# Optimization experiments

Hardware: AMD Instinct MI355X
Metric: run time of the kernel (lower is better)

Reference implementation:

```python
import jax, jax.numpy as jnp
import numpy as np

N_HEADS, D_MODEL, D_HEAD = 16, 1024, 64
BATCH, SEQ = 2, 2048
INIT_RANGE = 0.02


def setup_inputs() -> dict:
    key = jax.random.key(0)
    ks = jax.random.split(key, 5)
    x = jax.random.normal(ks[0], (BATCH, SEQ, D_MODEL), dtype=jnp.float32)
    W_Q = jax.random.normal(ks[1], (N_HEADS, D_MODEL, D_HEAD), dtype=jnp.float32) * INIT_RANGE
    W_K = jax.random.normal(ks[2], (N_HEADS, D_MODEL, D_HEAD), dtype=jnp.float32) * INIT_RANGE
    W_V = jax.random.normal(ks[3], (N_HEADS, D_MODEL, D_HEAD), dtype=jnp.float32) * INIT_RANGE
    W_O = jax.random.normal(ks[4], (N_HEADS, D_HEAD, D_MODEL), dtype=jnp.float32) * INIT_RANGE
    b_Q = jnp.zeros((N_HEADS, D_HEAD), dtype=jnp.float32)
    b_K = jnp.zeros((N_HEADS, D_HEAD), dtype=jnp.float32)
    b_V = jnp.zeros((N_HEADS, D_HEAD), dtype=jnp.float32)
    b_O = jnp.zeros((D_MODEL,), dtype=jnp.float32)
    return {"normalized_resid_pre": x, "W_Q": W_Q, "W_K": W_K, "W_V": W_V,
            "W_O": W_O, "b_Q": b_Q, "b_K": b_K, "b_V": b_V, "b_O": b_O}


def reference(normalized_resid_pre, W_Q, W_K, W_V, W_O, b_Q, b_K, b_V, b_O):
    x = normalized_resid_pre  # [b, s, d_model]
    q = jnp.einsum('bsm,hmd->bshd', x, W_Q) + b_Q  # [b, s, h, d_head]
    k = jnp.einsum('bsm,hmd->bshd', x, W_K) + b_K
    v = jnp.einsum('bsm,hmd->bshd', x, W_V) + b_V
    scores = jnp.einsum('bqhd,bkhd->bhqk', q, k) / jnp.sqrt(jnp.float32(D_HEAD))
    seq = x.shape[1]
    causal = jnp.tril(jnp.ones((seq, seq), dtype=bool))  # True where allowed
    scores = jnp.where(causal, scores, jnp.float32(-jnp.inf))
    pattern = jax.nn.softmax(scores, axis=-1)  # [b, h, q, k]
    z = jnp.einsum('bhqk,bkhd->bqhd', pattern, v)
    attn_out = jnp.einsum('bqhd,hdm->bqm', z, W_O) + b_O
    return attn_out
```

## Files before the change

kernel.cpp:

```cpp
#include <hip/hip_runtime.h>
#include <hip/hip_bf16.h>

#define BATCH 2
#define SEQL 2048
#define NH 16
#define DH 64
#define DM 1024
#define QSCALE 0.1803368801111244f

typedef __hip_bfloat16 bf16;
typedef __attribute__((ext_vector_type(8)))  short bf16x8;
typedef __attribute__((ext_vector_type(4)))  float f32x4;
typedef __attribute__((ext_vector_type(16))) float f32x16;

__device__ __forceinline__ void gl_lds16(const void* g, void* l) {
    __builtin_amdgcn_global_load_lds(
        (const __attribute__((address_space(1))) unsigned int*)g,
        (__attribute__((address_space(3))) unsigned int*)l, 16, 0, 0);
}

__device__ __forceinline__ unsigned int pkbf(float a, float b) {
    union { bf16 h[2]; unsigned int u; } x;
    x.h[0] = __float2bfloat16(a); x.h[1] = __float2bfloat16(b);
    return x.u;
}

__global__ __launch_bounds__(256) void prep_kernel(
    const float* __restrict__ x,
    const float* __restrict__ Wq, const float* __restrict__ Wk,
    const float* __restrict__ Wv, const float* __restrict__ Wo,
    bf16* __restrict__ Wt, bf16* __restrict__ xb)
{
    const int zi = blockIdx.z;
    if (zi == 4) {
        const int bid = blockIdx.y * 16 + blockIdx.x;
        const size_t base = ((size_t)bid * 256 + threadIdx.x) * 4;
        #pragma unroll
        for (int it = 0; it < 16; ++it) {
            const size_t i = base + (size_t)it * 262144;
            const float4 v = *(const float4*)(x + i);
            bf16 o[4];
            o[0] = __float2bfloat16(v.x); o[1] = __float2bfloat16(v.y);
            o[2] = __float2bfloat16(v.z); o[3] = __float2bfloat16(v.w);
            *(uint2*)(xb + i) = *(const uint2*)o;
        }
        return;
    }

    __shared__ float ts[64][65];
    const float* src = (zi == 0) ? Wq : (zi == 1) ? Wk : (zi == 2) ? Wv : Wo;
    bf16* dst = Wt + (size_t)zi * DM * DM;
    const int row0 = blockIdx.y * 64;
    const int col0 = blockIdx.x * 64;
    const int tx = threadIdx.x & 63;
    const int ty = threadIdx.x >> 6;

    if (zi < 3) {
        const int h = col0 >> 6;
        #pragma unroll
        for (int i = 0; i < 16; ++i) {
            const int r = ty + 4 * i;
            ts[r][tx] = src[h * (DM * DH) + (row0 + r) * DH + tx];
        }
    } else {
        #pragma unroll
        for (int i = 0; i < 16; ++i) {
            const int r = ty + 4 * i;
            ts[r][tx] = src[(size_t)(row0 + r) * DM + col0 + tx];
        }
    }
    __syncthreads();
    #pragma unroll
    for (int i = 0; i < 16; ++i) {
        const int rr = ty + 4 * i;
        dst[(size_t)(col0 + rr) * DM + row0 + tx] = __float2bfloat16(ts[tx][rr]);
    }
}

__global__ __launch_bounds__(256) void qkv_gemm(
    const bf16* __restrict__ xb, const bf16* __restrict__ Wt,
    const float* __restrict__ bq, const float* __restrict__ bk, const float* __restrict__ bv,
    bf16* __restrict__ qkv)
{
    __shared__ __align__(16) bf16 As[2][128 * 32];
    __shared__ __align__(16) bf16 Bs[2][128 * 32];

    const int t = threadIdx.x;
    const int lane = t & 63, w = t >> 6;
    const int ml = lane & 15, quad = lane >> 4;
    const int wr = w >> 1, wc = w & 1;
    const int bn = blockIdx.x, bm = blockIdx.y, which = blockIdx.z;

    const bf16* A0 = xb + (size_t)(bm * 128) * DM;
    const bf16* B0 = Wt + (size_t)which * DM * DM + (size_t)(bn * 128) * DM;
    const float* bias = (which == 0) ? bq : (which == 1) ? bk : bv;
    bf16* outb = qkv + (size_t)which * (BATCH * SEQL * NH * DH);
    const float oscale = (which == 0) ? QSCALE : 1.0f;

    f32x4 acc[4][4];
    #pragma unroll
    for (int i = 0; i < 4; ++i)
        #pragma unroll
        for (int j = 0; j < 4; ++j) acc[i][j] = (f32x4){0.f, 0.f, 0.f, 0.f};

    const int r0 = t >> 2, c0 = (t & 3) * 8;
    const int f1 = t + 256;
    const int r1 = f1 >> 2, c1 = (f1 & 3) * 8;

    for (int kt = 0; kt < DM / 64; ++kt) {
        const int k0 = kt * 64;
        __syncthreads();
        #pragma unroll
        for (int half = 0; half < 2; ++half) {
            const int kh = k0 + half * 32;
            gl_lds16(A0 + (size_t)r0 * DM + kh + c0, &As[half][t * 8]);
            gl_lds16(A0 + (size_t)r1 * DM + kh + c1, &As[half][f1 * 8]);
            gl_lds16(B0 + (size_t)r0 * DM + kh + c0, &Bs[half][t * 8]);
            gl_lds16(B0 + (size_t)r1 * DM + kh + c1, &Bs[half][f1 * 8]);
        }
        __syncthreads();
        #pragma unroll
        for (int half = 0; half < 2; ++half) {
            bf16x8 af[4], bfr[4];
            #pragma unroll
            for (int i = 0; i < 4; ++i)
                af[i] = *(const bf16x8*)&As[half][(wr * 64 + i * 16 + ml) * 32 + quad * 8];
            #pragma unroll
            for (int j = 0; j < 4; ++j)
                bfr[j] = *(const bf16x8*)&Bs[half][(wc * 64 + j * 16 + ml) * 32 + quad * 8];
            #pragma unroll
            for (int i = 0; i < 4; ++i)
                #pragma unroll
                for (int j = 0; j < 4; ++j)
                    acc[i][j] = __builtin_amdgcn_mfma_f32_16x16x32_bf16(af[i], bfr[j], acc[i][j], 0, 0, 0);
        }
    }

    float bb[4];
    #pragma unroll
    for (int j = 0; j < 4; ++j) bb[j] = bias[bn * 128 + wc * 64 + j * 16 + ml];

    if (which == 2) {
        #pragma unroll
        for (int i = 0; i < 4; ++i) {
            const int row0v = bm * 128 + wr * 64 + i * 16 + quad * 4;
            const int b = row0v >> 11;
            const int s0 = row0v & (SEQL - 1);
            #pragma unroll
            for (int j = 0; j < 4; ++j) {
                const int col = bn * 128 + wc * 64 + j * 16 + ml;
                const int h = col >> 6, d = col & 63;
                bf16 tmp[4];
                #pragma unroll
                for (int rg = 0; rg < 4; ++rg)
                    tmp[rg] = __float2bfloat16(acc[i][j][rg] + bb[j]);
                *(uint2*)&outb[(((size_t)(b * NH + h)) * DH + d) * SEQL + s0] =
                    *(const uint2*)tmp;
            }
        }
    } else {
        #pragma unroll
        for (int i = 0; i < 4; ++i) {
            #pragma unroll
            for (int rg = 0; rg < 4; ++rg) {
                const int row = bm * 128 + wr * 64 + i * 16 + quad * 4 + rg;
                const int b = row >> 11;
                const int s = row & (SEQL - 1);
                #pragma unroll
                for (int j = 0; j < 4; ++j) {
                    const int col = bn * 128 + wc * 64 + j * 16 + ml;
                    const int h = col >> 6, d = col & 63;
                    outb[(((size_t)(b * NH + h)) * SEQL + s) * DH + d] =
                        __float2bfloat16((acc[i][j][rg] + bb[j]) * oscale);
                }
            }
        }
    }
}

__global__ __launch_bounds__(256) void oproj_gemm(
    const bf16* __restrict__ zb, const bf16* __restrict__ Bt,
    const float* __restrict__ bo, float* __restrict__ out)
{
    __shared__ __align__(16) bf16 As[2][128 * 32];
    __shared__ __align__(16) bf16 Bs[2][64 * 32];

    const int t = threadIdx.x;
    const int lane = t & 63, w = t >> 6;
    const int ml = lane & 15, quad = lane >> 4;
    const int wr = w >> 1, wc = w & 1;
    const int bn = blockIdx.x, bm = blockIdx.y;

    const bf16* A0 = zb + (size_t)(bm * 128) * DM;
    const bf16* B0 = Bt + (size_t)(bn * 64) * DM;

    f32x4 acc[4][2];
    #pragma unroll
    for (int i = 0; i < 4; ++i)
        #pragma unroll
        for (int j = 0; j < 2; ++j) acc[i][j] = (f32x4){0.f, 0.f, 0.f, 0.f};

    const int r0 = t >> 2, c0 = (t & 3) * 8;
    const int f1 = t + 256;
    const int r1 = f1 >> 2, c1 = (f1 & 3) * 8;

    for (int kt = 0; kt < DM / 64; ++kt) {
        const int k0 = kt * 64;
        __syncthreads();
        #pragma unroll
        for (int half = 0; half < 2; ++half) {
            const int kh = k0 + half * 32;
            gl_lds16(A0 + (size_t)r0 * DM + kh + c0, &As[half][t * 8]);
            gl_lds16(A0 + (size_t)r1 * DM + kh + c1, &As[half][f1 * 8]);
            gl_lds16(B0 + (size_t)r0 * DM + kh + c0, &Bs[half][t * 8]);
        }
        __syncthreads();
        #pragma unroll
        for (int half = 0; half < 2; ++half) {
            bf16x8 af[4], bfr[2];
            #pragma unroll
            for (int i = 0; i < 4; ++i)
                af[i] = *(const bf16x8*)&As[half][(wr * 64 + i * 16 + ml) * 32 + quad * 8];
            #pragma unroll
            for (int j = 0; j < 2; ++j)
                bfr[j] = *(const bf16x8*)&Bs[half][(wc * 32 + j * 16 + ml) * 32 + quad * 8];
            #pragma unroll
            for (int i = 0; i < 4; ++i)
                #pragma unroll
                for (int j = 0; j < 2; ++j)
                    acc[i][j] = __builtin_amdgcn_mfma_f32_16x16x32_bf16(af[i], bfr[j], acc[i][j], 0, 0, 0);
        }
    }

    float bb[2];
    #pragma unroll
    for (int j = 0; j < 2; ++j) bb[j] = bo[bn * 64 + wc * 32 + j * 16 + ml];

    #pragma unroll
    for (int i = 0; i < 4; ++i) {
        #pragma unroll
        for (int rg = 0; rg < 4; ++rg) {
            const int row = bm * 128 + wr * 64 + i * 16 + quad * 4 + rg;
            #pragma unroll
            for (int j = 0; j < 2; ++j) {
                const int col = bn * 64 + wc * 32 + j * 16 + ml;
                out[(size_t)row * DM + col] = acc[i][j][rg] + bb[j];
            }
        }
    }
}

__global__ __launch_bounds__(256) void attn_kernel(
    const bf16* __restrict__ qg, const bf16* __restrict__ kg, const bf16* __restrict__ vtg,
    bf16* __restrict__ z)
{
    __shared__ __align__(16) bf16 KsS[2][64 * 64];
    __shared__ __align__(16) bf16 VtS[2][64 * 64];

    const int t    = threadIdx.x;
    const int lane = t & 63;
    const int w    = t >> 6;
    const int q5   = lane & 31;
    const int hl   = lane >> 5;
    const int qgr  = w & 1;
    const int kvg  = w >> 1;

    const int bh = blockIdx.x;
    const int b  = bh >> 4;
    const int h  = bh & 15;
    const int qt = (gridDim.y - 1) - blockIdx.y;
    const int q0 = qt * 64;

    const size_t base   = (size_t)bh * SEQL * DH;
    const size_t vtbase = (size_t)bh * DH * SEQL;

    const int s0 = t, s1 = t + 256;
    const int r0s = s0 >> 3, c0s = (s0 & 7) ^ (r0s & 7);
    const int r1s = s1 >> 3, c1s = (s1 & 7) ^ (r1s & 7);

    bf16x8 aq[4];
    {
        const bf16* qp = qg + base + (size_t)(q0 + qgr * 32 + q5) * DH;
        #pragma unroll
        for (int c = 0; c < 4; ++c)
            aq[c] = *(const bf16x8*)(qp + c * 16 + hl * 8);
    }

    f32x16 zacc[2];
    #pragma unroll
    for (int dg = 0; dg < 2; ++dg)
        #pragma unroll
        for (int r = 0; r < 16; ++r) zacc[dg][r] = 0.f;
    float lacc = 0.f;

    gl_lds16(kg + base + (size_t)r0s * DH + c0s * 8, &KsS[0][s0 * 8]);
    gl_lds16(kg + base + (size_t)r1s * DH + c1s * 8, &KsS[0][s1 * 8]);
    gl_lds16(vtg + vtbase + (size_t)r0s * SEQL + c0s * 8, &VtS[0][s0 * 8]);
    gl_lds16(vtg + vtbase + (size_t)r1s * SEQL + c1s * 8, &VtS[0][s1 * 8]);

    for (int kt = 0; kt <= qt; ++kt) {
        const int cur = kt & 1;
        __syncthreads();

        if (kt < qt) {
            const int kc = (kt + 1) * 64;
            bf16* Kd = &KsS[cur ^ 1][0];
            bf16* Vd = &VtS[cur ^ 1][0];
            gl_lds16(kg + base + (size_t)(kc + r0s) * DH + c0s * 8, Kd + s0 * 8);
            gl_lds16(kg + base + (size_t)(kc + r1s) * DH + c1s * 8, Kd + s1 * 8);
            gl_lds16(vtg + vtbase + (size_t)r0s * SEQL + kc + c0s * 8, Vd + s0 * 8);
            gl_lds16(vtg + vtbase + (size_t)r1s * SEQL + kc + c1s * 8, Vd + s1 * 8);
        }

        if (kt == qt && kvg == 1 && qgr == 0) continue;

        const bf16* Ks = &KsS[cur][0];
        const bf16* Vt = &VtS[cur][0];

        f32x16 sc;
        #pragma unroll
        for (int r = 0; r < 16; ++r) sc[r] = 0.f;
        {
            const int row = kvg * 32 + q5;
            const int rx  = row & 7;
            __builtin_amdgcn_s_setprio(1);
            #pragma unroll
            for (int s = 0; s < 4; ++s) {
                const int cc = (s * 2 + hl) ^ rx;
                const bf16x8 ak = *(const bf16x8*)(&Ks[row * 64 + cc * 8]);
                sc = __builtin_amdgcn_mfma_f32_32x32x16_bf16(ak, aq[s], sc, 0, 0, 0);
            }
            __builtin_amdgcn_s_setprio(0);
        }

        if (kt == qt && kvg == qgr) {
            #pragma unroll
            for (int r = 0; r < 16; ++r) {
                const int kvloc = (r & 3) + 8 * (r >> 2) + 4 * hl;
                sc[r] = (kvloc > q5) ? -1e30f : sc[r];
            }
        }

        unsigned int wpk[8];
        #pragma unroll
        for (int g = 0; g < 4; ++g) {
            const float p0 = __builtin_exp2f(sc[4 * g + 0]);
            const float p1 = __builtin_exp2f(sc[4 * g + 1]);
            const float p2 = __builtin_exp2f(sc[4 * g + 2]);
            const float p3 = __builtin_exp2f(sc[4 * g + 3]);
            lacc += (p0 + p1) + (p2 + p3);
            wpk[2 * g + 0] = pkbf(p0, p1);
            wpk[2 * g + 1] = pkbf(p2, p3);
        }

        bf16x8 pf[2];
        #pragma unroll
        for (int ks = 0; ks < 2; ++ks) {
            const unsigned int S0 = hl ? wpk[4 * ks + 0] : wpk[4 * ks + 2];
            const unsigned int S1 = hl ? wpk[4 * ks + 1] : wpk[4 * ks + 3];
            const unsigned int R0 = __shfl_xor((int)S0, 32);
            const unsigned int R1 = __shfl_xor((int)S1, 32);
            union { unsigned int u[4]; bf16x8 v; } f;
            f.u[0] = hl ? R0 : wpk[4 * ks + 0];
            f.u[1] = hl ? R1 : wpk[4 * ks + 1];
            f.u[2] = hl ? wpk[4 * ks + 2] : R0;
            f.u[3] = hl ? wpk[4 * ks + 3] : R1;
            pf[ks] = f.v;
        }

        __builtin_amdgcn_s_setprio(1);
        #pragma unroll
        for (int dg = 0; dg < 2; ++dg) {
            const int row = dg * 32 + q5;
            const int rx  = row & 7;
            #pragma unroll
            for (int ks = 0; ks < 2; ++ks) {
                const int cc = (kvg * 4 + ks * 2 + hl) ^ rx;
                const bf16x8 av = *(const bf16x8*)(&Vt[row * 64 + cc * 8]);
                zacc[dg] = __builtin_amdgcn_mfma_f32_32x32x16_bf16(av, pf[ks], zacc[dg], 0, 0, 0);
            }
        }
        __builtin_amdgcn_s_setprio(0);
    }

    __syncthreads();
    if (kvg == 1) {
        float* sp = (qgr == 0) ? (float*)KsS : (float*)VtS;
        #pragma unroll
        for (int dg = 0; dg < 2; ++dg)
            #pragma unroll
            for (int r = 0; r < 16; ++r)
                sp[(dg * 16 + r) * 64 + lane] = zacc[dg][r];
        sp[2048 + lane] = lacc;
    }
    __syncthreads();
    if (kvg == 0) {
        const float* sp = (qgr == 0) ? (const float*)KsS : (const float*)VtS;
        #pragma unroll
        for (int dg = 0; dg < 2; ++dg)
            #pragma unroll
            for (int r = 0; r < 16; ++r)
                zacc[dg][r] += sp[(dg * 16 + r) * 64 + lane];
        lacc += sp[2048 + lane];
        lacc += __shfl_xor(lacc, 32);
        const float invl = 1.f / lacc;

        const int qrow = q0 + qgr * 32 + q5;
        bf16* zp = z + (((size_t)b * SEQL + qrow) * NH + h) * DH;
        #pragma unroll
        for (int dg = 0; dg < 2; ++dg) {
            #pragma unroll
            for (int g2 = 0; g2 < 4; ++g2) {
                bf16 tmp[4];
                #pragma unroll
                for (int j = 0; j < 4; ++j)
                    tmp[j] = __float2bfloat16(zacc[dg][4 * g2 + j] * invl);
                *(uint2*)(zp + dg * 32 + 8 * g2 + 4 * hl) = *(const uint2*)tmp;
            }
        }
    }
}

extern "C" void kernel_launch(void* const* d_in, const int* in_sizes, int n_in,
                              void* d_out, int out_size, void* d_ws, size_t ws_size,
                              hipStream_t stream)
{
    const float* x  = (const float*)d_in[0];
    const float* Wq = (const float*)d_in[1];
    const float* Wk = (const float*)d_in[2];
    const float* Wv = (const float*)d_in[3];
    const float* Wo = (const float*)d_in[4];
    const float* bq = (const float*)d_in[5];
    const float* bk = (const float*)d_in[6];
    const float* bv = (const float*)d_in[7];
    const float* bo = (const float*)d_in[8];
    float* out = (float*)d_out;

    const size_t TOK = (size_t)BATCH * SEQL;
    const size_t QKV = TOK * DM;
    bf16* xb  = (bf16*)d_ws;
    bf16* Wt  = xb + QKV;
    bf16* qkv = Wt + 4 * (size_t)DM * DM;
    bf16* zb  = qkv + 3 * QKV;

    prep_kernel<<<dim3(16, 16, 5), 256, 0, stream>>>(x, Wq, Wk, Wv, Wo, Wt, xb);
    qkv_gemm<<<dim3(8, 32, 3), 256, 0, stream>>>(xb, Wt, bq, bk, bv, qkv);
    attn_kernel<<<dim3(BATCH * NH, SEQL / 64), 256, 0, stream>>>(
        qkv, qkv + QKV, qkv + 2 * QKV, zb);
    oproj_gemm<<<dim3(16, 32), 256, 0, stream>>>(zb, Wt + 3 * (size_t)DM * DM, bo, out);
}
```

Baseline: 183.3 us.

## Restructure attention blocks to 32 queries with 4-way KV split over 128-key tiles

Each attention block now handles 32 query rows instead of 64, and its four waves each take a 32-key slice of a 128-key tile, so the grid doubles and the work split across waves changes. The row-sum of probabilities is computed with an MFMA against a ones matrix instead of scalar adds. K/V staging becomes single-buffered 128-key tiles with a wider swizzle for V. Partial results from waves 1-3 are reduced through LDS by wave 0. This gives more parallelism and fewer loop iterations, but drops the double-buffered prefetch, so load latency is exposed, and waves sit idle on the causal diagonal tiles.

```diff
diff --git a/kernel.cpp b/kernel.cpp
--- a/kernel.cpp
+++ b/kernel.cpp
@@ -254,159 +254,159 @@
     const bf16* __restrict__ qg, const bf16* __restrict__ kg, const bf16* __restrict__ vtg,
     bf16* __restrict__ z)
 {
-    __shared__ __align__(16) bf16 KsS[2][64 * 64];
-    __shared__ __align__(16) bf16 VtS[2][64 * 64];
+    __shared__ __align__(16) bf16 SM[128 * 64 + 64 * 128];
+    bf16* Ks = SM;
+    bf16* Vt = SM + 128 * 64;
 
     const int t    = threadIdx.x;
     const int lane = t & 63;
     const int w    = t >> 6;
     const int q5   = lane & 31;
     const int hl   = lane >> 5;
-    const int qgr  = w & 1;
-    const int kvg  = w >> 1;
 
     const int bh = blockIdx.x;
     const int b  = bh >> 4;
     const int h  = bh & 15;
-    const int qt = (gridDim.y - 1) - blockIdx.y;
-    const int q0 = qt * 64;
+    const int qt = 63 - (int)blockIdx.y;
+    const int q0 = qt * 32;
+    const int iters = (qt >> 2) + 1;
 
     const size_t base   = (size_t)bh * SEQL * DH;
     const size_t vtbase = (size_t)bh * DH * SEQL;
 
-    const int s0 = t, s1 = t + 256;
-    const int r0s = s0 >> 3, c0s = (s0 & 7) ^ (r0s & 7);
-    const int r1s = s1 >> 3, c1s = (s1 & 7) ^ (r1s & 7);
+    int krow[4], kcol[4], vrow[4], vcol[4];
+    #pragma unroll
+    for (int i = 0; i < 4; ++i) {
+        const int s = t + 256 * i;
+        krow[i] = s >> 3;  kcol[i] = (s & 7)  ^ (krow[i] & 7);
+        vrow[i] = s >> 4;  vcol[i] = (s & 15) ^ (vrow[i] & 15);
+    }
 
     bf16x8 aq[4];
     {
-        const bf16* qp = qg + base + (size_t)(q0 + qgr * 32 + q5) * DH;
-        #pragma unroll
-        for (int c = 0; c < 4; ++c)
-            aq[c] = *(const bf16x8*)(qp + c * 16 + hl * 8);
-    }
+        const bf16* qp = qg + base + (size_t)(q0 + q5) * DH;
+        #pragma unroll
+        for (int s = 0; s < 4; ++s)
+            aq[s] = *(const bf16x8*)(qp + s * 16 + hl * 8);
+    }
+
+    const short o1 = (short)0x3F80;
+    const bf16x8 onesA = {o1, o1, o1, o1, o1, o1, o1, o1};
 
     f32x16 zacc[2];
     #pragma unroll
     for (int dg = 0; dg < 2; ++dg)
         #pragma unroll
         for (int r = 0; r < 16; ++r) zacc[dg][r] = 0.f;
-    float lacc = 0.f;
-
-    gl_lds16(kg + base + (size_t)r0s * DH + c0s * 8, &KsS[0][s0 * 8]);
-    gl_lds16(kg + base + (size_t)r1s * DH + c1s * 8, &KsS[0][s1 * 8]);
-    gl_lds16(vtg + vtbase + (size_t)r0s * SEQL + c0s * 8, &VtS[0][s0 * 8]);
-    gl_lds16(vtg + vtbase + (size_t)r1s * SEQL + c1s * 8, &VtS[0][s1 * 8]);
-
-    for (int kt = 0; kt <= qt; ++kt) {
-        const int cur = kt & 1;
+    f32x16 laccv;
+    #pragma unroll
+    for (int r = 0; r < 16; ++r) laccv[r] = 0.f;
+
+    for (int it = 0; it < iters; ++it) {
+        const int kc = it * 128;
+        if (it) __syncthreads();
+        #pragma unroll
+        for (int i = 0; i < 4; ++i) {
+            gl_lds16(kg + base + (size_t)(kc + krow[i]) * DH + kcol[i] * 8,
+                     &Ks[(t + 256 * i) * 8]);
+            gl_lds16(vtg + vtbase + (size_t)vrow[i] * SEQL + kc + vcol[i] * 8,
+                     &Vt[(t + 256 * i) * 8]);
+        }
         __syncthreads();
 
-        if (kt < qt) {
-            const int kc = (kt + 1) * 64;
-            bf16* Kd = &KsS[cur ^ 1][0];
-            bf16* Vd = &VtS[cur ^ 1][0];
-            gl_lds16(kg + base + (size_t)(kc + r0s) * DH + c0s * 8, Kd + s0 * 8);
-            gl_lds16(kg + base + (size_t)(kc + r1s) * DH + c1s * 8, Kd + s1 * 8);
-            gl_lds16(vtg + vtbase + (size_t)r0s * SEQL + kc + c0s * 8, Vd + s0 * 8);
-            gl_lds16(vtg + vtbase + (size_t)r1s * SEQL + kc + c1s * 8, Vd + s1 * 8);
-        }
-
-        if (kt == qt && kvg == 1 && qgr == 0) continue;
-
-        const bf16* Ks = &KsS[cur][0];
-        const bf16* Vt = &VtS[cur][0];
-
-        f32x16 sc;
-        #pragma unroll
-        for (int r = 0; r < 16; ++r) sc[r] = 0.f;
-        {
-            const int row = kvg * 32 + q5;
-            const int rx  = row & 7;
+        const int kvbase = kc + w * 32;
+        if (kvbase <= q0 + 31) {
+            f32x16 sc;
+            #pragma unroll
+            for (int r = 0; r < 16; ++r) sc[r] = 0.f;
+            {
+                const int krw = w * 32 + q5;
+                const int krx = krw & 7;
+                __builtin_amdgcn_s_setprio(1);
+                #pragma unroll
+                for (int s = 0; s < 4; ++s) {
+                    const int cc = (s * 2 + hl) ^ krx;
+                    const bf16x8 ak = *(const bf16x8*)(&Ks[krw * 64 + cc * 8]);
+                    sc = __builtin_amdgcn_mfma_f32_32x32x16_bf16(ak, aq[s], sc, 0, 0, 0);
+                }
+                __builtin_amdgcn_s_setprio(0);
+            }
+
+            if (it == iters - 1 && kvbase + 31 > q0) {
+                #pragma unroll
+                for (int r = 0; r < 16; ++r) {
+                    const int kvloc = (r & 3) + 8 * (r >> 2) + 4 * hl;
+                    sc[r] = (kvbase + kvloc > q0 + q5) ? -1e30f : sc[r];
+                }
+            }
+
+            unsigned int wpk[8];
+            #pragma unroll
+            for (int g = 0; g < 4; ++g) {
+                const float p0 = __builtin_exp2f(sc[4 * g + 0]);
+                const float p1 = __builtin_exp2f(sc[4 * g + 1]);
+                const float p2 = __builtin_exp2f(sc[4 * g + 2]);
+                const float p3 = __builtin_exp2f(sc[4 * g + 3]);
+                wpk[2 * g + 0] = pkbf(p0, p1);
+                wpk[2 * g + 1] = pkbf(p2, p3);
+            }
+
+            bf16x8 pf[2];
+            #pragma unroll
+            for (int ks = 0; ks < 2; ++ks) {
+                const unsigned int S0 = hl ? wpk[4 * ks + 0] : wpk[4 * ks + 2];
+                const unsigned int S1 = hl ? wpk[4 * ks + 1] : wpk[4 * ks + 3];
+                const unsigned int R0 = __shfl_xor((int)S0, 32);
+                const unsigned int R1 = __shfl_xor((int)S1, 32);
+                union { unsigned int u[4]; bf16x8 v; } f;
+                f.u[0] = hl ? R0 : wpk[4 * ks + 0];
+                f.u[1] = hl ? R1 : wpk[4 * ks + 1];
+                f.u[2] = hl ? wpk[4 * ks + 2] : R0;
+                f.u[3] = hl ? wpk[4 * ks + 3] : R1;
+                pf[ks] = f.v;
+            }
+
             __builtin_amdgcn_s_setprio(1);
             #pragma unroll
-            for (int s = 0; s < 4; ++s) {
-                const int cc = (s * 2 + hl) ^ rx;
-                const bf16x8 ak = *(const bf16x8*)(&Ks[row * 64 + cc * 8]);
-                sc = __builtin_amdgcn_mfma_f32_32x32x16_bf16(ak, aq[s], sc, 0, 0, 0);
+            for (int ks = 0; ks < 2; ++ks) {
+                laccv = __builtin_amdgcn_mfma_f32_32x32x16_bf16(onesA, pf[ks], laccv, 0, 0, 0);
+                #pragma unroll
+                for (int dg = 0; dg < 2; ++dg) {
+                    const int row = dg * 32 + q5;
+                    const int cc  = (w * 4 + ks * 2 + hl) ^ (row & 15);
+                    const bf16x8 av = *(const bf16x8*)(&Vt[row * 128 + cc * 8]);
+                    zacc[dg] = __builtin_amdgcn_mfma_f32_32x32x16_bf16(av, pf[ks], zacc[dg], 0, 0, 0);
+                }
             }
             __builtin_amdgcn_s_setprio(0);
         }
-
-        if (kt == qt && kvg == qgr) {
-            #pragma unroll
-            for (int r = 0; r < 16; ++r) {
-                const int kvloc = (r & 3) + 8 * (r >> 2) + 4 * hl;
-                sc[r] = (kvloc > q5) ? -1e30f : sc[r];
-            }
-        }
-
-        unsigned int wpk[8];
-        #pragma unroll
-        for (int g = 0; g < 4; ++g) {
-            const float p0 = __builtin_exp2f(sc[4 * g + 0]);
-            const float p1 = __builtin_exp2f(sc[4 * g + 1]);
-            const float p2 = __builtin_exp2f(sc[4 * g + 2]);
-            const float p3 = __builtin_exp2f(sc[4 * g + 3]);
-            lacc += (p0 + p1) + (p2 + p3);
-            wpk[2 * g + 0] = pkbf(p0, p1);
-            wpk[2 * g + 1] = pkbf(p2, p3);
-        }
-
-        bf16x8 pf[2];
-        #pragma unroll
-        for (int ks = 0; ks < 2; ++ks) {
-            const unsigned int S0 = hl ? wpk[4 * ks + 0] : wpk[4 * ks + 2];
-            const unsigned int S1 = hl ? wpk[4 * ks + 1] : wpk[4 * ks + 3];
-            const unsigned int R0 = __shfl_xor((int)S0, 32);
-            const unsigned int R1 = __shfl_xor((int)S1, 32);
-            union { unsigned int u[4]; bf16x8 v; } f;
-            f.u[0] = hl ? R0 : wpk[4 * ks + 0];
-            f.u[1] = hl ? R1 : wpk[4 * ks + 1];
-            f.u[2] = hl ? wpk[4 * ks + 2] : R0;
-            f.u[3] = hl ? wpk[4 * ks + 3] : R1;
-            pf[ks] = f.v;
-        }
-
-        __builtin_amdgcn_s_setprio(1);
-        #pragma unroll
-        for (int dg = 0; dg < 2; ++dg) {
-            const int row = dg * 32 + q5;
-            const int rx  = row & 7;
-            #pragma unroll
-            for (int ks = 0; ks < 2; ++ks) {
-                const int cc = (kvg * 4 + ks * 2 + hl) ^ rx;
-                const bf16x8 av = *(const bf16x8*)(&Vt[row * 64 + cc * 8]);
-                zacc[dg] = __builtin_amdgcn_mfma_f32_32x32x16_bf16(av, pf[ks], zacc[dg], 0, 0, 0);
-            }
-        }
-        __builtin_amdgcn_s_setprio(0);
     }
 
     __syncthreads();
-    if (kvg == 1) {
-        float* sp = (qgr == 0) ? (float*)KsS : (float*)VtS;
+    float* sp = (float*)SM;
+    if (w > 0) {
+        float* zp = sp + (size_t)(w - 1) * 2048;
         #pragma unroll
         for (int dg = 0; dg < 2; ++dg)
             #pragma unroll
             for (int r = 0; r < 16; ++r)
-                sp[(dg * 16 + r) * 64 + lane] = zacc[dg][r];
-        sp[2048 + lane] = lacc;
+                zp[(dg * 16 + r) * 64 + lane] = zacc[dg][r];
+        sp[6144 + (w - 1) * 64 + lane] = laccv[0];
     }
     __syncthreads();
-    if (kvg == 0) {
-        const float* sp = (qgr == 0) ? (const float*)KsS : (const float*)VtS;
-        #pragma unroll
-        for (int dg = 0; dg < 2; ++dg)
-            #pragma unroll
-            for (int r = 0; r < 16; ++r)
-                zacc[dg][r] += sp[(dg * 16 + r) * 64 + lane];
-        lacc += sp[2048 + lane];
-        lacc += __shfl_xor(lacc, 32);
-        const float invl = 1.f / lacc;
-
-        const int qrow = q0 + qgr * 32 + q5;
-        bf16* zp = z + (((size_t)b * SEQL + qrow) * NH + h) * DH;
+    if (w == 0) {
+        #pragma unroll
+        for (int p = 0; p < 3; ++p)
+            #pragma unroll
+            for (int dg = 0; dg < 2; ++dg)
+                #pragma unroll
+                for (int r = 0; r < 16; ++r)
+                    zacc[dg][r] += sp[p * 2048 + (dg * 16 + r) * 64 + lane];
+        const float l = laccv[0] + sp[6144 + lane] + sp[6144 + 64 + lane]
+                                 + sp[6144 + 128 + lane];
+        const float invl = 1.f / l;
+
+        bf16* zp = z + (((size_t)b * SEQL + q0 + q5) * NH + h) * DH;
         #pragma unroll
         for (int dg = 0; dg < 2; ++dg) {
             #pragma unroll
@@ -445,7 +445,7 @@
 
     prep_kernel<<<dim3(16, 16, 5), 256, 0, stream>>>(x, Wq, Wk, Wv, Wo, Wt, xb);
     qkv_gemm<<<dim3(8, 32, 3), 256, 0, stream>>>(xb, Wt, bq, bk, bv, qkv);
-    attn_kernel<<<dim3(BATCH * NH, SEQL / 64), 256, 0, stream>>>(
+    attn_kernel<<<dim3(BATCH * NH, SEQL / 32), 256, 0, stream>>>(
         qkv, qkv + QKV, qkv + 2 * QKV, zb);
     oproj_gemm<<<dim3(16, 32), 256, 0, stream>>>(zb, Wt + 3 * (size_t)DM * DM, bo, out);
 }
```

New measurement: 199.2 us. 8.7% more time.
